# Performance work log

Hardware: AMD Instinct MI355X
Metric: run time of the kernel (lower is better)

## Reference

```python
import jax, jax.numpy as jnp
import numpy as np

N_HEAD = 16
HEAD_DIM = 128
HIDDEN = 2048
ROPE_BASE = 10000.0
RMS_EPS = 1e-5


def _rms_norm(t, w, eps=RMS_EPS):
    # RMSNorm over last dim with learned scale
    var = jnp.mean(jnp.square(t), axis=-1, keepdims=True)
    return t * jax.lax.rsqrt(var + eps) * w


def _rope_cos_sin(T, dim, base=ROPE_BASE, dtype=jnp.float32):
    inv_freq = 1.0 / (base ** (jnp.arange(0, dim, 2, dtype=jnp.float32) / dim))
    pos = jnp.arange(T, dtype=jnp.float32)
    freqs = pos[:, None] * inv_freq[None, :]  # [T, dim/2]
    return jnp.cos(freqs).astype(dtype), jnp.sin(freqs).astype(dtype)


def _apply_rotary(t, cos, sin):
    # t: [B, T, H, D]; rotate-half (GPT-NeoX style)
    d2 = t.shape[-1] // 2
    t1, t2 = t[..., :d2], t[..., d2:]
    c = cos[None, :, None, :]
    s = sin[None, :, None, :]
    return jnp.concatenate([t1 * c - t2 * s, t1 * s + t2 * c], axis=-1)


def setup_inputs() -> dict:
    key = jax.random.key(0)
    ks = jax.random.split(key, 7)
    B, T = 2, 2048
    w_std = 1.0 / np.sqrt(HIDDEN)
    proj_std = 0.5 / np.sqrt(HIDDEN) / np.sqrt(24)  # hidden_init_std_factor / sqrt(H) / sqrt(L)
    return {
        "x": jax.random.normal(ks[0], (B, T, HIDDEN), jnp.float32),
        "Wq": jax.random.normal(ks[1], (HIDDEN, N_HEAD * HEAD_DIM), jnp.float32) * w_std,
        "Wk": jax.random.normal(ks[2], (HIDDEN, N_HEAD * HEAD_DIM), jnp.float32) * w_std,
        "Wv": jax.random.normal(ks[3], (HIDDEN, N_HEAD * HEAD_DIM), jnp.float32) * w_std,
        "Wg": jax.random.normal(ks[4], (HIDDEN, N_HEAD * HEAD_DIM), jnp.float32) * w_std,
        "Wo": jax.random.normal(ks[5], (N_HEAD * HEAD_DIM, HIDDEN), jnp.float32) * proj_std,
        "q_rms_w": jnp.ones((HEAD_DIM,), jnp.float32),
        "k_rms_w": jnp.ones((HEAD_DIM,), jnp.float32),
        "o_norm_w": jnp.ones((HEAD_DIM,), jnp.float32),
    }


def reference(x, Wq, Wk, Wv, Wg, Wo, q_rms_w, k_rms_w, o_norm_w):
    B, T, _ = x.shape
    H, D = N_HEAD, HEAD_DIM

    q = (x @ Wq).reshape(B, T, H, D)
    k = (x @ Wk).reshape(B, T, H, D)
    v = (x @ Wv).reshape(B, T, H, D)

    # RoPE (no past, offset = 0)
    cos, sin = _rope_cos_sin(T, D, dtype=x.dtype)
    q = _apply_rotary(q, cos, sin)
    k = _apply_rotary(k, cos, sin)

    # QK RMSNorm (per-head-dim affine)
    q = _rms_norm(q, q_rms_w)
    k = _rms_norm(k, k_rms_w)

    # causal SDPA
    scale = 1.0 / np.sqrt(D)
    scores = jnp.einsum("bqhd,bkhd->bhqk", q, k) * scale
    causal = jnp.tril(jnp.ones((T, T), dtype=bool))
    scores = jnp.where(causal[None, None, :, :], scores, jnp.finfo(scores.dtype).min)
    probs = jax.nn.softmax(scores, axis=-1)
    y = jnp.einsum("bhqk,bkhd->bqhd", probs, v)  # [B, T, H, D]

    # output norm + silu gate
    y = _rms_norm(y, o_norm_w)
    gate = (x @ Wg).reshape(B, T, H, D)
    y = y * jax.nn.silu(gate)

    y = y.reshape(B, T, H * D)
    return y @ Wo
```

## Files before the change

### kernel.cpp

```cpp
#include <hip/hip_runtime.h>
#include <hip/hip_bf16.h>
#include <stdint.h>

typedef __bf16 bf16x8 __attribute__((ext_vector_type(8)));
typedef float f32x4 __attribute__((ext_vector_type(4)));
typedef __hip_bfloat16 bf16;

__device__ __forceinline__ void gload16(const void* g, void* l) {
    __builtin_amdgcn_global_load_lds(
        (const __attribute__((address_space(1))) uint32_t*)g,
        (__attribute__((address_space(3))) uint32_t*)l,
        16, 0, 0);
}

__global__ void k_cvt_bf16(const float* __restrict__ in, bf16* __restrict__ out, int n4) {
    int i = blockIdx.x * blockDim.x + threadIdx.x;
    if (i >= n4) return;
    float4 v = reinterpret_cast<const float4*>(in)[i];
    union { bf16 h[4]; uint2 u; } pk;
    pk.h[0] = __float2bfloat16(v.x);
    pk.h[1] = __float2bfloat16(v.y);
    pk.h[2] = __float2bfloat16(v.z);
    pk.h[3] = __float2bfloat16(v.w);
    reinterpret_cast<uint2*>(out)[i] = pk.u;
}

__global__ void k_rope_tbl(float* __restrict__ tbl) {
    int i = blockIdx.x * blockDim.x + threadIdx.x;
    int t = i >> 6, j = i & 63;
    float inv = powf(10000.0f, -(float)j * (1.0f / 64.0f));
    float f = (float)t * inv;
    tbl[t * 128 + j] = cosf(f);
    tbl[t * 128 + 64 + j] = sinf(f);
}

__global__ void k_wtrans(const float* __restrict__ w0, const float* __restrict__ w1,
                         const float* __restrict__ w2, const float* __restrict__ w3,
                         const float* __restrict__ w4, bf16* __restrict__ out) {
    __shared__ float tile[64][65];
    const float* srcs[5] = {w0, w1, w2, w3, w4};
    const float* src = srcs[blockIdx.z];
    bf16* dst = out + (size_t)blockIdx.z * 2048 * 2048;
    int k0 = blockIdx.x * 64, n0 = blockIdx.y * 64;
    int tx = threadIdx.x, ty = threadIdx.y;
#pragma unroll
    for (int i = 0; i < 16; i++)
        tile[ty + 4 * i][tx] = src[(size_t)(k0 + ty + 4 * i) * 2048 + n0 + tx];
    __syncthreads();
#pragma unroll
    for (int i = 0; i < 16; i++)
        dst[(size_t)(n0 + ty + 4 * i) * 2048 + k0 + tx] = __float2bfloat16(tile[tx][ty + 4 * i]);
}

__global__ __launch_bounds__(256) void k_gemm(
    const bf16* __restrict__ A, const bf16* __restrict__ Bt, float* __restrict__ C,
    int M, int N, int K) {
    __shared__ __align__(16) bf16 As[128 * 64];
    __shared__ __align__(16) bf16 Bs[128 * 64];
    int lane = threadIdx.x & 63, wave = threadIdx.x >> 6;
    int g = lane >> 4, cc = lane & 15;
    int wr = wave >> 1, wc = wave & 1;
    size_t m0 = (size_t)blockIdx.x * 128, n0 = (size_t)blockIdx.y * 128;
    const bf16* Ab = A + m0 * K;
    const bf16* Bb = Bt + (size_t)blockIdx.z * N * K + n0 * K;
    float* Cb = C + (size_t)blockIdx.z * M * N + m0 * N + n0;

    f32x4 acc[4][4];
#pragma unroll
    for (int i = 0; i < 4; i++)
#pragma unroll
        for (int j = 0; j < 4; j++) acc[i][j] = {0.f, 0.f, 0.f, 0.f};

    int scol = (lane & 7) * 8;
    for (int k0 = 0; k0 < K; k0 += 64) {
#pragma unroll
        for (int i = 0; i < 4; i++) {
            int ch = wave * 4 + i;
            int row = ch * 8 + (lane >> 3);
            gload16(&Ab[(size_t)row * K + k0 + scol], &As[ch * 512]);
            gload16(&Bb[(size_t)row * K + k0 + scol], &Bs[ch * 512]);
        }
        __syncthreads();
#pragma unroll
        for (int kk = 0; kk < 2; kk++) {
            bf16x8 af[4], bfr[4];
#pragma unroll
            for (int m = 0; m < 4; m++)
                af[m] = *reinterpret_cast<const bf16x8*>(&As[(wr * 64 + m * 16 + cc) * 64 + kk * 32 + g * 8]);
#pragma unroll
            for (int n = 0; n < 4; n++)
                bfr[n] = *reinterpret_cast<const bf16x8*>(&Bs[(wc * 64 + n * 16 + cc) * 64 + kk * 32 + g * 8]);
#pragma unroll
            for (int m = 0; m < 4; m++)
#pragma unroll
                for (int n = 0; n < 4; n++)
                    acc[m][n] = __builtin_amdgcn_mfma_f32_16x16x32_bf16(af[m], bfr[n], acc[m][n], 0, 0, 0);
        }
        __syncthreads();
    }
#pragma unroll
    for (int m = 0; m < 4; m++)
#pragma unroll
        for (int n = 0; n < 4; n++)
#pragma unroll
            for (int r = 0; r < 4; r++) {
                size_t row = wr * 64 + m * 16 + g * 4 + r;
                Cb[row * N + (wc * 64 + n * 16 + cc)] = acc[m][n][r];
            }
}

__global__ __launch_bounds__(512, 2) void k_gemm256(
    const bf16* __restrict__ A, const bf16* __restrict__ Bt, bf16* __restrict__ C,
    int M, int N, int K) {
    __shared__ __align__(16) bf16 lds[2][8][64 * 64];
    const int tid = threadIdx.x;
    const int lane = tid & 63, wave = tid >> 6;
    const int g = lane >> 4, c = lane & 15, cx = c & 7;
    const int wr = wave >> 2, wc = wave & 3;
    const int id = blockIdx.x;
    const int swz = (id & 7) * 64 + (id >> 3);
    const int xt = swz & 15, yt = (swz >> 4) & 7, zt = swz >> 7;
    const size_t m0 = (size_t)xt * 256, n0 = (size_t)yt * 256;
    const bf16* Ab = A + m0 * K;
    const bf16* Bb = Bt + (size_t)zt * (size_t)N * K + n0 * K;
    bf16* Cb = C + (size_t)zt * (size_t)M * N + m0 * N + n0;
    const int nt = K >> 6;

    const int srow = tid >> 3;
    const int scol = ((tid & 7) ^ (srow & 7)) * 8;

    auto stage = [&](int u, int q) {
        if (u >= nt) return;
        const bf16* src = (q < 4) ? &Ab[(size_t)(q * 64 + srow) * K]
                                  : &Bb[(size_t)((q - 4) * 64 + srow) * K];
        gload16(&src[((size_t)u << 6) + scol], &lds[u & 1][q][wave * 512]);
    };

    f32x4 acc[8][4];
#pragma unroll
    for (int i = 0; i < 8; i++)
#pragma unroll
        for (int j = 0; j < 4; j++) acc[i][j] = {0.f, 0.f, 0.f, 0.f};

#pragma unroll
    for (int q = 0; q < 8; q++) stage(0, q);
    stage(1, 0); stage(1, 2); stage(1, 4); stage(1, 5); stage(1, 6); stage(1, 7);
    asm volatile("s_waitcnt vmcnt(6)" ::: "memory");
    __builtin_amdgcn_s_barrier();

    bf16x8 afr[4][2], bfr[2][2][2];

#define READ_A(mh)                                                                   \
    do {                                                                             \
        const bf16* aq = &lds[t & 1][wr * 2 + (mh)][0];                              \
        _Pragma("unroll") for (int m_ = 0; m_ < 4; m_++)                             \
            _Pragma("unroll") for (int kh = 0; kh < 2; kh++)                         \
                afr[m_][kh] = *reinterpret_cast<const bf16x8*>(                      \
                    aq + (m_ * 16 + c) * 64 + ((kh * 4 + g) ^ cx) * 8);              \
    } while (0)
#define READ_B(nh)                                                                   \
    do {                                                                             \
        const bf16* bq = &lds[t & 1][4 + wc][0];                                     \
        _Pragma("unroll") for (int n_ = 0; n_ < 2; n_++)                             \
            _Pragma("unroll") for (int kh = 0; kh < 2; kh++)                         \
                bfr[nh][n_][kh] = *reinterpret_cast<const bf16x8*>(                  \
                    bq + (((nh)*2 + n_) * 16 + c) * 64 + ((kh * 4 + g) ^ cx) * 8);   \
    } while (0)
#define QUAD(mh, nh)                                                                 \
    do {                                                                             \
        __builtin_amdgcn_s_setprio(1);                                               \
        _Pragma("unroll") for (int kh = 0; kh < 2; kh++)                             \
            _Pragma("unroll") for (int m_ = 0; m_ < 4; m_++)                         \
                _Pragma("unroll") for (int n_ = 0; n_ < 2; n_++)                     \
                    acc[(mh)*4 + m_][(nh)*2 + n_] =                                  \
                        __builtin_amdgcn_mfma_f32_16x16x32_bf16(                     \
                            afr[m_][kh], bfr[nh][n_][kh],                            \
                            acc[(mh)*4 + m_][(nh)*2 + n_], 0, 0, 0);                 \
        __builtin_amdgcn_s_setprio(0);                                               \
    } while (0)

    for (int t = 0; t < nt; ++t) {
        READ_A(0);
        READ_B(0);
        stage(t + 1, 1); stage(t + 1, 3);
        QUAD(0, 0);
        __builtin_amdgcn_s_barrier();
        READ_B(1);
        stage(t + 2, 0); stage(t + 2, 2);
        QUAD(0, 1);
        __builtin_amdgcn_s_barrier();
        READ_A(1);
        stage(t + 2, 4); stage(t + 2, 5);
        QUAD(1, 0);
        __builtin_amdgcn_s_barrier();
        stage(t + 2, 6); stage(t + 2, 7);
        if (t < nt - 2) asm volatile("s_waitcnt vmcnt(6)" ::: "memory");
        else            asm volatile("s_waitcnt vmcnt(0)" ::: "memory");
        QUAD(1, 1);
        __builtin_amdgcn_s_barrier();
    }
#undef READ_A
#undef READ_B
#undef QUAD
#pragma unroll
    for (int m_ = 0; m_ < 8; m_++)
#pragma unroll
        for (int n_ = 0; n_ < 4; n_++)
#pragma unroll
            for (int r_ = 0; r_ < 4; r_++) {
                size_t row = wr * 128 + m_ * 16 + g * 4 + r_;
                Cb[row * N + wc * 64 + n_ * 16 + c] = __float2bfloat16(acc[m_][n_][r_]);
            }
}

__global__ void k_rope_rms(const bf16* __restrict__ src_q, const bf16* __restrict__ src_k,
                           const float* __restrict__ qw, const float* __restrict__ kw,
                           const float* __restrict__ tbl, bf16* __restrict__ dst_q,
                           bf16* __restrict__ dst_k) {
    const int T = 2048;
    int role = blockIdx.y;
    const bf16* src = role ? src_k : src_q;
    const float* rmsw = role ? kw : qw;
    bf16* dst = role ? dst_k : dst_q;
    float outscale = role ? 1.0f : 0.08838834764831845f;
    int wv = blockIdx.x * 4 + (threadIdx.x >> 6);
    int lane = threadIdx.x & 63;
    int hq = wv & 3, bt = wv >> 2;
    int t = bt & (T - 1), b_ = bt >> 11;
    int hsub = lane >> 4;
    int half = (lane >> 3) & 1;
    int jj = (lane & 7) * 8;

    bf16x8 v = *reinterpret_cast<const bf16x8*>(
        src + (size_t)bt * 2048 + hq * 512 + lane * 8);
    float f[8], g[8];
#pragma unroll
    for (int j = 0; j < 8; j++) f[j] = (float)v[j];
#pragma unroll
    for (int j = 0; j < 8; j++) g[j] = __shfl_xor(f[j], 8, 64);

    const float* tb = tbl + t * 128;
    float4 c0 = *reinterpret_cast<const float4*>(&tb[jj]);
    float4 c1 = *reinterpret_cast<const float4*>(&tb[jj + 4]);
    float4 s0 = *reinterpret_cast<const float4*>(&tb[64 + jj]);
    float4 s1 = *reinterpret_cast<const float4*>(&tb[64 + jj + 4]);
    float cs[8] = {c0.x, c0.y, c0.z, c0.w, c1.x, c1.y, c1.z, c1.w};
    float sn[8] = {s0.x, s0.y, s0.z, s0.w, s1.x, s1.y, s1.z, s1.w};

    float out[8];
    float ssum = 0.f;
#pragma unroll
    for (int j = 0; j < 8; j++) {
        float a = half ? g[j] : f[j];
        float b = half ? f[j] : g[j];
        float o = half ? (a * sn[j] + b * cs[j]) : (a * cs[j] - b * sn[j]);
        out[j] = o;
        ssum += o * o;
    }
    ssum += __shfl_xor(ssum, 1, 64);
    ssum += __shfl_xor(ssum, 2, 64);
    ssum += __shfl_xor(ssum, 4, 64);
    ssum += __shfl_xor(ssum, 8, 64);
    float rs = rsqrtf(ssum * (1.0f / 128.0f) + 1e-5f) * outscale;

    int d0 = half * 64 + jj;
    float4 w0 = *reinterpret_cast<const float4*>(&rmsw[d0]);
    float4 w1 = *reinterpret_cast<const float4*>(&rmsw[d0 + 4]);
    float wv8[8] = {w0.x, w0.y, w0.z, w0.w, w1.x, w1.y, w1.z, w1.w};
    union { bf16 h[8]; uint4 u; } pk;
#pragma unroll
    for (int j = 0; j < 8; j++) pk.h[j] = __float2bfloat16(out[j] * rs * wv8[j]);
    int h = hq * 4 + hsub;
    size_t o = ((size_t)(b_ * 16 + h) * T + t) * 128 + d0;
    *reinterpret_cast<uint4*>(dst + o) = pk.u;
}

__global__ void k_vtrans(const bf16* __restrict__ V, bf16* __restrict__ Vt) {
    const int T = 2048;
    __shared__ float tile[64][65];
    int bh = blockIdx.z, b_ = bh >> 4, h = bh & 15;
    int t0 = blockIdx.x * 64, d0 = blockIdx.y * 64;
    int tx = threadIdx.x, ty = threadIdx.y;
#pragma unroll
    for (int i = 0; i < 16; i++)
        tile[ty + 4 * i][tx] =
            __bfloat162float(V[((size_t)(b_ * T + t0 + ty + 4 * i)) * 2048 + h * 128 + d0 + tx]);
    __syncthreads();
#pragma unroll
    for (int i = 0; i < 16; i++)
        Vt[((size_t)bh * 128 + d0 + ty + 4 * i) * T + t0 + tx] = __float2bfloat16(tile[tx][ty + 4 * i]);
}

__global__ __launch_bounds__(256) void k_attn(
    const bf16* __restrict__ Q, const bf16* __restrict__ K,
    const bf16* __restrict__ Vt, const bf16* __restrict__ gate,
    const float* __restrict__ ow, bf16* __restrict__ out) {
    const int T = 2048;
    __shared__ __align__(16) bf16 KsB[2][64 * 128];
    __shared__ __align__(16) bf16 VsB[2][128 * 64];
    int lane = threadIdx.x & 63, wave = threadIdx.x >> 6;
    int g = lane >> 4, c = lane & 15;
    int wg = blockIdx.x;
    int bh = wg & 31;
    int qt = 31 - (wg >> 5);
    int q0 = qt * 64;
    const bf16* Qb = Q + (size_t)bh * T * 128;
    const bf16* Kb = K + (size_t)bh * T * 128;
    const bf16* Vb = Vt + (size_t)bh * 128 * T;

    int qrow = q0 + wave * 16 + c;
    bf16x8 qf[4];
#pragma unroll
    for (int kk = 0; kk < 4; kk++)
        qf[kk] = *reinterpret_cast<const bf16x8*>(&Qb[(size_t)qrow * 128 + kk * 32 + g * 8]);

    int kprow[4], klu[4], vrow[4], vlu[4];
#pragma unroll
    for (int i = 0; i < 4; i++) {
        int ch = wave * 4 + i;
        int p = ch * 4 + (lane >> 4);
        kprow[i] = ((p >> 5) & 1) * 32 + ((p >> 2) & 3) * 8 + ((p >> 4) & 1) * 4 + (p & 3);
        klu[i] = (lane & 15) ^ (p & 7);
        vrow[i] = ch * 8 + (lane >> 3);
        vlu[i] = (lane & 7) ^ (vrow[i] & 7);
    }
    auto stage = [&](int kv0, int b) {
#pragma unroll
        for (int i = 0; i < 4; i++) {
            int ch = wave * 4 + i;
            gload16(&Kb[(size_t)(kv0 + kprow[i]) * 128 + klu[i] * 8], &KsB[b][ch * 512]);
            gload16(&Vb[(size_t)vrow[i] * T + kv0 + vlu[i] * 8], &VsB[b][ch * 512]);
        }
    };

    f32x4 acc[8];
#pragma unroll
    for (int i = 0; i < 8; i++) acc[i] = {0.f, 0.f, 0.f, 0.f};
    float m = -INFINITY, l = 0.f;

    int ntiles = qt + 1;
    stage(0, 0);
    __syncthreads();
    int cur = 0;
    for (int it = 0; it < ntiles; ++it) {
        int kv0 = it * 64;
        if (it + 1 < ntiles) stage(kv0 + 64, cur ^ 1);
        const bf16* Ks = KsB[cur];
        const bf16* Vs = VsB[cur];

        f32x4 s[4];
#pragma unroll
        for (int nf = 0; nf < 4; nf++) s[nf] = {0.f, 0.f, 0.f, 0.f};
#pragma unroll
        for (int nf = 0; nf < 4; nf++)
#pragma unroll
            for (int kk = 0; kk < 4; kk++) {
                int pu = (kk * 4 + g) ^ (c & 7);
                bf16x8 kf = *reinterpret_cast<const bf16x8*>(&Ks[(nf * 16 + c) * 128 + pu * 8]);
                s[nf] = __builtin_amdgcn_mfma_f32_16x16x32_bf16(kf, qf[kk], s[nf], 0, 0, 0);
            }
        if (it == ntiles - 1) {
#pragma unroll
            for (int nf = 0; nf < 4; nf++)
#pragma unroll
                for (int r = 0; r < 4; r++)
                    if (kv0 + (nf >> 1) * 32 + g * 8 + (nf & 1) * 4 + r > qrow)
                        s[nf][r] = -1e30f;
        }
        float mx = -INFINITY;
#pragma unroll
        for (int nf = 0; nf < 4; nf++)
#pragma unroll
            for (int r = 0; r < 4; r++) mx = fmaxf(mx, s[nf][r]);
        mx = fmaxf(mx, __shfl_xor(mx, 16, 64));
        mx = fmaxf(mx, __shfl_xor(mx, 32, 64));
        if (__all(mx - m <= 8.0f)) {
            float rsum = 0.f;
#pragma unroll
            for (int nf = 0; nf < 4; nf++)
#pragma unroll
                for (int r = 0; r < 4; r++) {
                    float p = __expf(s[nf][r] - m);
                    s[nf][r] = p;
                    rsum += p;
                }
            rsum += __shfl_xor(rsum, 16, 64);
            rsum += __shfl_xor(rsum, 32, 64);
            l += rsum;
        } else {
            float mnew = fmaxf(m, mx);
            float alpha = __expf(m - mnew);
            m = mnew;
            float rsum = 0.f;
#pragma unroll
            for (int nf = 0; nf < 4; nf++)
#pragma unroll
                for (int r = 0; r < 4; r++) {
                    float p = __expf(s[nf][r] - mnew);
                    s[nf][r] = p;
                    rsum += p;
                }
            rsum += __shfl_xor(rsum, 16, 64);
            rsum += __shfl_xor(rsum, 32, 64);
            l = l * alpha + rsum;
            float al[4];
#pragma unroll
            for (int r = 0; r < 4; r++) al[r] = __shfl(alpha, g * 4 + r, 64);
#pragma unroll
            for (int nf = 0; nf < 8; nf++)
#pragma unroll
                for (int r = 0; r < 4; r++) acc[nf][r] *= al[r];
        }
#pragma unroll
        for (int kk2 = 0; kk2 < 2; kk2++) {
            union { bf16 h[8]; bf16x8 v; } pf;
#pragma unroll
            for (int r = 0; r < 4; r++) {
                pf.h[r] = __float2bfloat16(s[2 * kk2][r]);
                pf.h[4 + r] = __float2bfloat16(s[2 * kk2 + 1][r]);
            }
#pragma unroll
            for (int nf = 0; nf < 8; nf++) {
                int pu = (kk2 * 4 + g) ^ (c & 7);
                bf16x8 vf = *reinterpret_cast<const bf16x8*>(&Vs[(nf * 16 + c) * 64 + pu * 8]);
                acc[nf] = __builtin_amdgcn_mfma_f32_16x16x32_bf16(pf.v, vf, acc[nf], 0, 0, 0);
            }
        }
        __syncthreads();
        cur ^= 1;
    }
    float inv = 1.0f / l;
    float iv[4];
#pragma unroll
    for (int r = 0; r < 4; r++) iv[r] = __shfl(inv, g * 4 + r, 64);
    int b_ = bh >> 4, h = bh & 15;
    float owv[8];
#pragma unroll
    for (int nf = 0; nf < 8; nf++) owv[nf] = ow[nf * 16 + c];
#pragma unroll
    for (int r = 0; r < 4; r++) {
        int row = q0 + wave * 16 + g * 4 + r;
        float y[8];
        float ss = 0.f;
#pragma unroll
        for (int nf = 0; nf < 8; nf++) {
            y[nf] = acc[nf][r] * iv[r];
            ss += y[nf] * y[nf];
        }
        ss += __shfl_xor(ss, 1, 64);
        ss += __shfl_xor(ss, 2, 64);
        ss += __shfl_xor(ss, 4, 64);
        ss += __shfl_xor(ss, 8, 64);
        float rs = rsqrtf(ss * (1.0f / 128.0f) + 1e-5f);
        size_t gi = ((size_t)(b_ * T + row)) * 2048 + h * 128;
#pragma unroll
        for (int nf = 0; nf < 8; nf++) {
            int col = nf * 16 + c;
            float gv = __bfloat162float(gate[gi + col]);
            gv = gv / (1.f + __expf(-gv));
            out[gi + col] = __float2bfloat16(y[nf] * rs * owv[nf] * gv);
        }
    }
}

extern "C" void kernel_launch(void* const* d_in, const int* in_sizes, int n_in,
                              void* d_out, int out_size, void* d_ws, size_t ws_size,
                              hipStream_t stream) {
    const float* x  = (const float*)d_in[0];
    const float* Wq = (const float*)d_in[1];
    const float* Wk = (const float*)d_in[2];
    const float* Wv = (const float*)d_in[3];
    const float* Wg = (const float*)d_in[4];
    const float* Wo = (const float*)d_in[5];
    const float* qw = (const float*)d_in[6];
    const float* kw = (const float*)d_in[7];
    const float* ow = (const float*)d_in[8];

    const size_t M = 4096, HID = 2048;
    char* w = (char*)d_ws;
    bf16*  xb    = (bf16*)(w);
    bf16*  Wt    = (bf16*)(w + 16777216);
    bf16*  qkvg  = (bf16*)(w + 58720256);
    bf16*  q_att = (bf16*)(w + 125829120);
    bf16*  k_att = (bf16*)(w + 142606336);
    bf16*  vt    = (bf16*)(w + 159383552);
    float* tbl   = (float*)(w + 176160768);
    bf16*  yg    = (bf16*)(w + 177209344);

    k_cvt_bf16<<<8192, 256, 0, stream>>>(x, xb, (int)(M * HID / 4));
    k_rope_tbl<<<512, 256, 0, stream>>>(tbl);
    k_wtrans<<<dim3(32, 32, 5), dim3(64, 4), 0, stream>>>(Wq, Wk, Wv, Wg, Wo, Wt);
    k_gemm256<<<512, 512, 0, stream>>>(xb, Wt, qkvg, (int)M, 2048, 2048);
    k_rope_rms<<<dim3(4096, 2), 256, 0, stream>>>(qkvg, qkvg + M * HID, qw, kw, tbl,
                                                  q_att, k_att);
    k_vtrans<<<dim3(32, 2, 32), dim3(64, 4), 0, stream>>>(qkvg + 2 * M * HID, vt);
    k_attn<<<1024, 256, 0, stream>>>(q_att, k_att, vt, qkvg + 3 * M * HID, ow, yg);
    k_gemm<<<dim3(32, 16, 1), 256, 0, stream>>>(yg, Wt + (size_t)4 * 2048 * 2048, (float*)d_out,
                                                (int)M, 2048, 2048);
}
```

Before: 304.7 us.

## Reuse 256-tile GEMM for output projection and merge pipeline phases

The separate 128x128 fp32-output GEMM used for the output projection is removed. The 256x256 pipelined kernel is templated on output type and launched with 128 blocks for that projection, with a block swizzle derived from the grid size. Inside the main loop the four compute phases per K-step are merged into two, and the B and A fragment reads are moved earlier, cutting the barriers per step from four to two. This lowers sync and LDS-read stalls, but 128 blocks cannot fill every CU on the device, and issuing the loads earlier raises register pressure.

After: 311.0 us. 2.1% more time.

```diff
diff --git a/kernel.cpp b/kernel.cpp
--- a/kernel.cpp
+++ b/kernel.cpp
@@ -52,78 +52,23 @@
         dst[(size_t)(n0 + ty + 4 * i) * 2048 + k0 + tx] = __float2bfloat16(tile[tx][ty + 4 * i]);
 }
 
-__global__ __launch_bounds__(256) void k_gemm(
-    const bf16* __restrict__ A, const bf16* __restrict__ Bt, float* __restrict__ C,
-    int M, int N, int K) {
-    __shared__ __align__(16) bf16 As[128 * 64];
-    __shared__ __align__(16) bf16 Bs[128 * 64];
-    int lane = threadIdx.x & 63, wave = threadIdx.x >> 6;
-    int g = lane >> 4, cc = lane & 15;
-    int wr = wave >> 1, wc = wave & 1;
-    size_t m0 = (size_t)blockIdx.x * 128, n0 = (size_t)blockIdx.y * 128;
-    const bf16* Ab = A + m0 * K;
-    const bf16* Bb = Bt + (size_t)blockIdx.z * N * K + n0 * K;
-    float* Cb = C + (size_t)blockIdx.z * M * N + m0 * N + n0;
-
-    f32x4 acc[4][4];
-#pragma unroll
-    for (int i = 0; i < 4; i++)
-#pragma unroll
-        for (int j = 0; j < 4; j++) acc[i][j] = {0.f, 0.f, 0.f, 0.f};
-
-    int scol = (lane & 7) * 8;
-    for (int k0 = 0; k0 < K; k0 += 64) {
-#pragma unroll
-        for (int i = 0; i < 4; i++) {
-            int ch = wave * 4 + i;
-            int row = ch * 8 + (lane >> 3);
-            gload16(&Ab[(size_t)row * K + k0 + scol], &As[ch * 512]);
-            gload16(&Bb[(size_t)row * K + k0 + scol], &Bs[ch * 512]);
-        }
-        __syncthreads();
-#pragma unroll
-        for (int kk = 0; kk < 2; kk++) {
-            bf16x8 af[4], bfr[4];
-#pragma unroll
-            for (int m = 0; m < 4; m++)
-                af[m] = *reinterpret_cast<const bf16x8*>(&As[(wr * 64 + m * 16 + cc) * 64 + kk * 32 + g * 8]);
-#pragma unroll
-            for (int n = 0; n < 4; n++)
-                bfr[n] = *reinterpret_cast<const bf16x8*>(&Bs[(wc * 64 + n * 16 + cc) * 64 + kk * 32 + g * 8]);
-#pragma unroll
-            for (int m = 0; m < 4; m++)
-#pragma unroll
-                for (int n = 0; n < 4; n++)
-                    acc[m][n] = __builtin_amdgcn_mfma_f32_16x16x32_bf16(af[m], bfr[n], acc[m][n], 0, 0, 0);
-        }
-        __syncthreads();
-    }
-#pragma unroll
-    for (int m = 0; m < 4; m++)
-#pragma unroll
-        for (int n = 0; n < 4; n++)
-#pragma unroll
-            for (int r = 0; r < 4; r++) {
-                size_t row = wr * 64 + m * 16 + g * 4 + r;
-                Cb[row * N + (wc * 64 + n * 16 + cc)] = acc[m][n][r];
-            }
-}
-
+template <typename OutT>
 __global__ __launch_bounds__(512, 2) void k_gemm256(
-    const bf16* __restrict__ A, const bf16* __restrict__ Bt, bf16* __restrict__ C,
+    const bf16* __restrict__ A, const bf16* __restrict__ Bt, OutT* __restrict__ C,
     int M, int N, int K) {
     __shared__ __align__(16) bf16 lds[2][8][64 * 64];
     const int tid = threadIdx.x;
     const int lane = tid & 63, wave = tid >> 6;
     const int g = lane >> 4, c = lane & 15, cx = c & 7;
     const int wr = wave >> 2, wc = wave & 3;
+    const int cpx = (int)gridDim.x >> 3;
     const int id = blockIdx.x;
-    const int swz = (id & 7) * 64 + (id >> 3);
+    const int swz = (id & 7) * cpx + (id >> 3);
     const int xt = swz & 15, yt = (swz >> 4) & 7, zt = swz >> 7;
     const size_t m0 = (size_t)xt * 256, n0 = (size_t)yt * 256;
     const bf16* Ab = A + m0 * K;
     const bf16* Bb = Bt + (size_t)zt * (size_t)N * K + n0 * K;
-    bf16* Cb = C + (size_t)zt * (size_t)M * N + m0 * N + n0;
+    OutT* Cb = C + (size_t)zt * (size_t)M * N + m0 * N + n0;
     const int nt = K >> 6;
 
     const int srow = tid >> 3;
@@ -182,20 +127,18 @@
     for (int t = 0; t < nt; ++t) {
         READ_A(0);
         READ_B(0);
+        READ_B(1);
         stage(t + 1, 1); stage(t + 1, 3);
         QUAD(0, 0);
-        __builtin_amdgcn_s_barrier();
-        READ_B(1);
-        stage(t + 2, 0); stage(t + 2, 2);
         QUAD(0, 1);
         __builtin_amdgcn_s_barrier();
         READ_A(1);
+        stage(t + 2, 0); stage(t + 2, 2);
         stage(t + 2, 4); stage(t + 2, 5);
-        QUAD(1, 0);
-        __builtin_amdgcn_s_barrier();
         stage(t + 2, 6); stage(t + 2, 7);
         if (t < nt - 2) asm volatile("s_waitcnt vmcnt(6)" ::: "memory");
         else            asm volatile("s_waitcnt vmcnt(0)" ::: "memory");
+        QUAD(1, 0);
         QUAD(1, 1);
         __builtin_amdgcn_s_barrier();
     }
@@ -209,7 +152,10 @@
 #pragma unroll
             for (int r_ = 0; r_ < 4; r_++) {
                 size_t row = wr * 128 + m_ * 16 + g * 4 + r_;
-                Cb[row * N + wc * 64 + n_ * 16 + c] = __float2bfloat16(acc[m_][n_][r_]);
+                if constexpr (sizeof(OutT) == 2)
+                    Cb[row * N + wc * 64 + n_ * 16 + c] = __float2bfloat16(acc[m_][n_][r_]);
+                else
+                    Cb[row * N + wc * 64 + n_ * 16 + c] = acc[m_][n_][r_];
             }
 }
 
@@ -490,11 +436,11 @@
     k_cvt_bf16<<<8192, 256, 0, stream>>>(x, xb, (int)(M * HID / 4));
     k_rope_tbl<<<512, 256, 0, stream>>>(tbl);
     k_wtrans<<<dim3(32, 32, 5), dim3(64, 4), 0, stream>>>(Wq, Wk, Wv, Wg, Wo, Wt);
-    k_gemm256<<<512, 512, 0, stream>>>(xb, Wt, qkvg, (int)M, 2048, 2048);
+    k_gemm256<bf16><<<512, 512, 0, stream>>>(xb, Wt, qkvg, (int)M, 2048, 2048);
     k_rope_rms<<<dim3(4096, 2), 256, 0, stream>>>(qkvg, qkvg + M * HID, qw, kw, tbl,
                                                   q_att, k_att);
     k_vtrans<<<dim3(32, 2, 32), dim3(64, 4), 0, stream>>>(qkvg + 2 * M * HID, vt);
     k_attn<<<1024, 256, 0, stream>>>(q_att, k_att, vt, qkvg + 3 * M * HID, ow, yg);
-    k_gemm<<<dim3(32, 16, 1), 256, 0, stream>>>(yg, Wt + (size_t)4 * 2048 * 2048, (float*)d_out,
-                                                (int)M, 2048, 2048);
-}
+    k_gemm256<float><<<128, 512, 0, stream>>>(yg, Wt + (size_t)4 * 2048 * 2048, (float*)d_out,
+                                              (int)M, 2048, 2048);
+}
```
